# Performance work log

Measured on AMD Instinct MI355X. Metric: run time of the kernel, lower is better.

The kernel has to match this reference:

```python
import jax, jax.numpy as jnp
import numpy as np

N = 4096
IN_F = 256
OUT_F = 64
H = 4
NEG_SLOPE = 0.2


def setup_inputs() -> dict:
    key = jax.random.key(0)
    k1, k2, k3, k4 = jax.random.split(key, 4)
    x = jax.random.normal(k1, (N, IN_F), dtype=jnp.float32)
    adj = jax.random.randint(k2, (N, N), 0, 2).astype(jnp.float32)
    # Xavier-uniform init, matching nn.init.xavier_uniform_
    limW = float(np.sqrt(6.0 / (IN_F + OUT_F)))
    W = jax.random.uniform(k3, (H, IN_F, OUT_F), minval=-limW, maxval=limW, dtype=jnp.float32)
    lima = float(np.sqrt(6.0 / (2 * OUT_F + 1)))
    a = jax.random.uniform(k4, (H, 2 * OUT_F, 1), minval=-lima, maxval=lima, dtype=jnp.float32)
    return {"x": x, "adj": adj, "W": W, "a": a}


def reference(x, adj, W, a):
    # x: [N, in], adj: [N, N], W: [H, in, out], a: [H, 2*out, 1]
    n = x.shape[0]
    h, _, fo = W.shape
    Wh = jnp.einsum('nd,hdo->nho', x, W)  # [N, H, O]
    # Additive score: a^T [Wh_i || Wh_j] = (a_src . Wh_i) + (a_dst . Wh_j)
    a_src = a[:, :fo, 0]   # [H, O]
    a_dst = a[:, fo:, 0]   # [H, O]
    s_i = jnp.einsum('nho,ho->nh', Wh, a_src)  # [N, H]
    s_j = jnp.einsum('nho,ho->nh', Wh, a_dst)  # [N, H]
    e = jax.nn.leaky_relu(s_i[:, None, :] + s_j[None, :, :], NEG_SLOPE)  # [N, N, H]
    # Add self-loops on the diagonal, mask non-edges
    idx = jnp.arange(n)
    adj_sl = adj.at[idx, idx].set(1.0)
    mask = (adj_sl != 0)[:, :, None]  # [N, N, 1]
    e_masked = jnp.where(mask, e, -jnp.inf)
    attention = jax.nn.softmax(e_masked, axis=1)  # softmax over neighbors j
    # (dropout is identity in eval mode)
    h_prime = jnp.einsum('ijh,jho->iho', attention, Wh)  # [N, H, O]
    return h_prime.reshape(n, h * fo)  # concat=True
```

## Files before the change

### kernel.cpp

```cpp
#include <hip/hip_runtime.h>
#include <hip/hip_bf16.h>

typedef float    f32x4 __attribute__((ext_vector_type(4)));
typedef _Float16 f16x8 __attribute__((ext_vector_type(8)));
typedef _Float16 f16x4 __attribute__((ext_vector_type(4)));
typedef __fp16   fp16x2 __attribute__((ext_vector_type(2)));

#define NN 4096
#define INF_ 256
#define OUTF 64
#define NH 4
#define NSPL 8
#define NGRP 128
#define LOG2E 1.4426950408889634f

__global__ __launch_bounds__(256) void k0_pack(const float* __restrict__ adj,
                                               unsigned* __restrict__ pack,
                                               unsigned* __restrict__ smax)
{
    const int r    = blockIdx.x;
    const int w    = threadIdx.x >> 6;
    const int lane = threadIdx.x & 63;
    const float* row = adj + (size_t)r * NN + w * 1024;
#pragma unroll
    for (int i = 0; i < 4; ++i) {
        float a0 = row[i*256 + lane];
        float a1 = row[i*256 +  64 + lane];
        float a2 = row[i*256 + 128 + lane];
        float a3 = row[i*256 + 192 + lane];
        unsigned long long bal[4];
        bal[0] = __ballot(a0 != 0.f);
        bal[1] = __ballot(a1 != 0.f);
        bal[2] = __ballot(a2 != 0.f);
        bal[3] = __ballot(a3 != 0.f);
        if (lane < 2) {
#pragma unroll
            for (int k = 0; k < 4; ++k) {
                int wi = w*32 + i*8 + k*2 + lane;
                unsigned v = (unsigned)(bal[k] >> (lane * 32));
                if (wi == (r >> 5)) v |= 1u << (r & 31);
                pack[r*128 + wi] = v;
            }
        }
    }
    if (r == 0 && threadIdx.x < NH) smax[threadIdx.x] = 0u;
}

__device__ __forceinline__ unsigned enc_f32(float f) {
    unsigned u = __float_as_uint(f);
    return (u & 0x80000000u) ? ~u : (u | 0x80000000u);
}
__device__ __forceinline__ float dec_f32(unsigned u) {
    return (u & 0x80000000u) ? __uint_as_float(u ^ 0x80000000u)
                             : __uint_as_float(~u);
}

__global__ __launch_bounds__(256) void kW_tr(const float* __restrict__ W,
                                             _Float16* __restrict__ wBh,
                                             _Float16* __restrict__ wBl)
{
    const int b = blockIdx.x;
    const int h = b >> 3, ks = b & 7;
    const int t = threadIdx.x;
    const int ob = t >> 6, lane = t & 63;
    const int row16 = lane & 15, quad = lane >> 4;

    const float* wp = W + (size_t)h*INF_*OUTF + (ks*32 + quad*8)*OUTF + ob*16 + row16;
    f16x8 vh, vl;
#pragma unroll
    for (int e = 0; e < 8; ++e) {
        float v = wp[e*OUTF];
        _Float16 hi = (_Float16)v;
        vh[e] = hi;
        vl[e] = (_Float16)(v - (float)hi);
    }
    const int idx = ((h*8 + ks)*4 + ob)*64 + lane;
    reinterpret_cast<f16x8*>(wBh)[idx] = vh;
    reinterpret_cast<f16x8*>(wBl)[idx] = vl;
}

__global__ __launch_bounds__(256) void k1m(
    const float* __restrict__ x, const _Float16* __restrict__ wBh,
    const _Float16* __restrict__ wBl, const float* __restrict__ a,
    _Float16* __restrict__ whB, float* __restrict__ s_src,
    float* __restrict__ s_dst, unsigned* __restrict__ smax)
{
    const int b = blockIdx.x;
    const int h = b >> 6, rb = b & 63;
    const int w = threadIdx.x >> 6, lane = threadIdx.x & 63;
    const int row16 = lane & 15, quad = lane >> 4;
    const int n0 = rb*64 + w*16;

    f32x4 acc[4];
#pragma unroll
    for (int ob = 0; ob < 4; ++ob) acc[ob] = (f32x4){0,0,0,0};

    const float* xp = x + (size_t)(n0 + row16)*INF_ + quad*8;
    const f16x8* WH = reinterpret_cast<const f16x8*>(wBh) + (h*8*4)*64 + lane;
    const f16x8* WL = reinterpret_cast<const f16x8*>(wBl) + (h*8*4)*64 + lane;

#pragma unroll
    for (int ks = 0; ks < 8; ++ks) {
        float4 xv0 = *reinterpret_cast<const float4*>(xp + ks*32);
        float4 xv1 = *reinterpret_cast<const float4*>(xp + ks*32 + 4);
        const float xv[8] = {xv0.x,xv0.y,xv0.z,xv0.w,xv1.x,xv1.y,xv1.z,xv1.w};
        f16x8 Ah, Al;
#pragma unroll
        for (int e = 0; e < 8; ++e) {
            _Float16 hi = (_Float16)xv[e];
            Ah[e] = hi;
            Al[e] = (_Float16)(xv[e] - (float)hi);
        }
#pragma unroll
        for (int ob = 0; ob < 4; ++ob) {
            f16x8 bh = WH[(ks*4 + ob)*64];
            f16x8 bl = WL[(ks*4 + ob)*64];
            acc[ob] = __builtin_amdgcn_mfma_f32_16x16x32_f16(Ah, bh, acc[ob], 0, 0, 0);
            acc[ob] = __builtin_amdgcn_mfma_f32_16x16x32_f16(Al, bh, acc[ob], 0, 0, 0);
            acc[ob] = __builtin_amdgcn_mfma_f32_16x16x32_f16(Ah, bl, acc[ob], 0, 0, 0);
        }
    }

    {
        const int jblk = n0 >> 5;
        const int qb   = ((n0 & 16) >> 3) + (quad >> 1);
        const int e0   = (quad & 1) * 4;
#pragma unroll
        for (int ob = 0; ob < 4; ++ob) {
            f16x4 st;
#pragma unroll
            for (int q = 0; q < 4; ++q) st[q] = (_Float16)acc[ob][q];
            const size_t off = (((size_t)(h*NGRP + jblk)*4 + ob)*64 + qb*16 + row16)*8 + e0;
            *reinterpret_cast<f16x4*>(whB + off) = st;
        }
    }

    float asv[4], adv[4];
#pragma unroll
    for (int ob = 0; ob < 4; ++ob) {
        asv[ob] = a[h*128 + ob*16 + row16];
        adv[ob] = a[h*128 + 64 + ob*16 + row16];
    }
    float sq_s[4], sq_d[4];
#pragma unroll
    for (int q = 0; q < 4; ++q) {
        float vs = 0.f, vd = 0.f;
#pragma unroll
        for (int ob = 0; ob < 4; ++ob) {
            vs += acc[ob][q] * asv[ob];
            vd += acc[ob][q] * adv[ob];
        }
#pragma unroll
        for (int m = 1; m <= 8; m <<= 1) {
            vs += __shfl_xor(vs, m);
            vd += __shfl_xor(vd, m);
        }
        sq_s[q] = vs; sq_d[q] = vd;
    }
    if (row16 == 0) {
        float vmax = -3.0e38f;
#pragma unroll
        for (int q = 0; q < 4; ++q) {
            const int n = n0 + quad*4 + q;
            s_src[h*NN + n] = LOG2E * sq_s[q];
            const float sd = LOG2E * sq_d[q];
            s_dst[h*NN + n] = sd;
            vmax = fmaxf(vmax, sd);
        }
        atomicMax(&smax[h], enc_f32(vmax));
    }
}

template <int USE_PART>
__global__ __launch_bounds__(256, 4) void k3_attn(
    const unsigned* __restrict__ pack, const _Float16* __restrict__ whB,
    const float* __restrict__ s_src, const float* __restrict__ s_dst,
    const unsigned* __restrict__ smax_enc,
    float* __restrict__ outp, float* __restrict__ l_ws)
{
    constexpr int STEPS_ = NN / NSPL / 32;

    const int b      = blockIdx.x;
    const int jsplit = b % NSPL;
    const int r2     = b / NSPL;
    const int hh     = r2 & 3;
    const int grp    = r2 >> 2;
    const int w      = threadIdx.x >> 6;
    const int lane   = threadIdx.x & 63;
    const int row16  = lane & 15;
    const int quad   = lane >> 4;
    const int i0     = (grp * 4 + w) * 32;
    const int jb0    = jsplit * (NN / NSPL);
    const int jblk0  = jb0 >> 5;

    const float sm = dec_f32(smax_enc[hh]);
    float A1[2], A2[2];
    const unsigned* prow[2];
#pragma unroll
    for (int f = 0; f < 2; ++f) {
        const int ir = i0 + f*16 + row16;
        const float s_i = s_src[hh*NN + ir];
        const float zb  = s_i + sm;
        const float mb  = fmaxf(zb, 0.2f * zb);
        A1[f] = s_i - mb;
        A2[f] = 0.2f * s_i - mb;
        prow[f] = pack + ir*128 + jblk0;
    }

    f32x4 acc[2][4];
    f32x4 accl[2];
#pragma unroll
    for (int f = 0; f < 2; ++f) {
        accl[f] = (f32x4){0,0,0,0};
#pragma unroll
        for (int ob = 0; ob < 4; ++ob) acc[f][ob] = (f32x4){0,0,0,0};
    }

    f16x8 ones;
#pragma unroll
    for (int e = 0; e < 8; ++e) ones[e] = (_Float16)1.0f;

    const _Float16* bB  = whB + (size_t)(hh*NGRP + jblk0)*2048 + lane*8;
    const float*    sdp = s_dst + hh*NN + jb0 + quad*8;

    f16x8 B0 = *reinterpret_cast<const f16x8*>(bB);
    f16x8 B1 = *reinterpret_cast<const f16x8*>(bB + 512);
    f16x8 B2 = *reinterpret_cast<const f16x8*>(bB + 1024);
    f16x8 B3 = *reinterpret_cast<const f16x8*>(bB + 1536);
    unsigned msk0 = prow[0][0], msk1 = prow[1][0];
    float4 sj0 = *reinterpret_cast<const float4*>(sdp);
    float4 sj1 = *reinterpret_cast<const float4*>(sdp + 4);

    for (int s = 0; s < STEPS_; ++s) {
        const _Float16* bn = bB + (s+1)*2048;
        f16x8 nB0 = *reinterpret_cast<const f16x8*>(bn);
        f16x8 nB1 = *reinterpret_cast<const f16x8*>(bn + 512);
        f16x8 nB2 = *reinterpret_cast<const f16x8*>(bn + 1024);
        f16x8 nB3 = *reinterpret_cast<const f16x8*>(bn + 1536);
        unsigned nmsk0 = prow[0][s+1], nmsk1 = prow[1][s+1];
        float4 nsj0 = *reinterpret_cast<const float4*>(sdp + (s+1)*32);
        float4 nsj1 = *reinterpret_cast<const float4*>(sdp + (s+1)*32 + 4);

        const float sjv[8] = {sj0.x,sj0.y,sj0.z,sj0.w,sj1.x,sj1.y,sj1.z,sj1.w};
        float us[8];
#pragma unroll
        for (int e = 0; e < 8; ++e) us[e] = 0.2f * sjv[e];

        const unsigned mskf[2] = {msk0, msk1};
#pragma unroll
        for (int f = 0; f < 2; ++f) {
            const unsigned mm8 = (mskf[f] >> (quad * 8)) & 0xffu;
            float pe[8];
#pragma unroll
            for (int e = 0; e < 8; ++e) {
                float t1 = A1[f] + sjv[e];
                float t2 = A2[f] + us[e];
                float p  = __builtin_amdgcn_exp2f(fmaxf(t1, t2));
                pe[e] = (mm8 & (1u << e)) ? p : 0.0f;
            }
            union { f16x8 v8; fp16x2 p2[4]; } pa;
#pragma unroll
            for (int e2 = 0; e2 < 4; ++e2)
                pa.p2[e2] = __builtin_amdgcn_cvt_pkrtz(pe[2*e2], pe[2*e2+1]);

            acc[f][0] = __builtin_amdgcn_mfma_f32_16x16x32_f16(pa.v8, B0, acc[f][0], 0, 0, 0);
            acc[f][1] = __builtin_amdgcn_mfma_f32_16x16x32_f16(pa.v8, B1, acc[f][1], 0, 0, 0);
            acc[f][2] = __builtin_amdgcn_mfma_f32_16x16x32_f16(pa.v8, B2, acc[f][2], 0, 0, 0);
            acc[f][3] = __builtin_amdgcn_mfma_f32_16x16x32_f16(pa.v8, B3, acc[f][3], 0, 0, 0);
            accl[f]   = __builtin_amdgcn_mfma_f32_16x16x32_f16(pa.v8, ones, accl[f], 0, 0, 0);
        }

        B0 = nB0; B1 = nB1; B2 = nB2; B3 = nB3;
        msk0 = nmsk0; msk1 = nmsk1;
        sj0 = nsj0; sj1 = nsj1;
    }

#pragma unroll
    for (int f = 0; f < 2; ++f) {
        if (row16 == 0) {
#pragma unroll
            for (int q = 0; q < 4; ++q) {
                const int ir = i0 + f*16 + quad*4 + q;
                if (USE_PART) l_ws[(jsplit*NH + hh)*NN + ir] = accl[f][q];
                else          atomicAdd(&l_ws[hh*NN + ir], accl[f][q]);
            }
        }
    }
    if (USE_PART) {
        float* pw = outp + ((size_t)((jsplit*NH + hh)*NGRP + (i0 >> 5))) * 2048 + lane;
#pragma unroll
        for (int f = 0; f < 2; ++f)
#pragma unroll
            for (int ob = 0; ob < 4; ++ob)
#pragma unroll
                for (int q = 0; q < 4; ++q)
                    pw[((f*4 + ob)*4 + q)*64] = acc[f][ob][q];
    } else {
#pragma unroll
        for (int f = 0; f < 2; ++f)
#pragma unroll
            for (int ob = 0; ob < 4; ++ob)
#pragma unroll
                for (int q = 0; q < 4; ++q) {
                    const int grow = i0 + f*16 + quad*4 + q;
                    const int gcol = hh*OUTF + ob*16 + row16;
                    atomicAdd(&outp[(size_t)grow*256 + gcol], acc[f][ob][q]);
                }
    }
}

__global__ __launch_bounds__(256) void k4_part(const float* __restrict__ part,
                                               const float* __restrict__ l_ws,
                                               float* __restrict__ out)
{
    const int idx = blockIdx.x * 256 + threadIdx.x;
    const int n = idx >> 6, c4 = idx & 63;
    const int h = c4 >> 4, k = c4 & 15;
    const int g = n >> 5, f = (n >> 4) & 1, quad = (n >> 2) & 3, q = n & 3;
    const int ob = k >> 2, lb = quad*16 + (k & 3)*4;

    float L = 0.f;
    f32x4 v = {0,0,0,0};
#pragma unroll
    for (int sp = 0; sp < NSPL; ++sp) {
        L += l_ws[(sp*NH + h)*NN + n];
        const float* p = part + ((size_t)((sp*NH + h)*NGRP + g))*2048
                              + ((f*4 + ob)*4 + q)*64 + lb;
        v += *reinterpret_cast<const f32x4*>(p);
    }
    const float inv = 1.0f / L;
    *reinterpret_cast<f32x4*>(out + (size_t)n*256 + c4*4) = v * inv;
}

__global__ __launch_bounds__(256) void k4_atomic(float* __restrict__ out,
                                                 const float* __restrict__ l_acc)
{
    const int idx = blockIdx.x * 256 + threadIdx.x;
    const int n = idx >> 6, c4 = idx & 63, h = c4 >> 4;
    const float inv = 1.0f / l_acc[h*NN + n];
    f32x4 v = *reinterpret_cast<f32x4*>(out + (size_t)n*256 + c4*4);
    *reinterpret_cast<f32x4*>(out + (size_t)n*256 + c4*4) = v * inv;
}

extern "C" void kernel_launch(void* const* d_in, const int* in_sizes, int n_in,
                              void* d_out, int out_size, void* d_ws, size_t ws_size,
                              hipStream_t stream)
{
    const float* x   = (const float*)d_in[0];
    const float* adj = (const float*)d_in[1];
    const float* W   = (const float*)d_in[2];
    const float* a   = (const float*)d_in[3];
    float* out = (float*)d_out;

    char* ws = (char*)d_ws;
    _Float16* whB  = (_Float16*)ws;
    unsigned* pack = (unsigned*)(ws + (2u<<20));
    _Float16* wBh  = (_Float16*)(ws + (4u<<20));
    _Float16* wBl  = (_Float16*)(ws + (4u<<20) + (128u<<10));
    float* s_src   = (float*)(ws + (4u<<20) + (256u<<10));
    float* s_dst   = (float*)(ws + (4u<<20) + (320u<<10));
    unsigned* smax = (unsigned*)(ws + (4u<<20) + (384u<<10));
    float* l_ws    = (float*)(ws + (4u<<20) + (385u<<10));
    float* part    = (float*)(ws + (4u<<20) + (897u<<10));

    const size_t need = (4u<<20) + (897u<<10) + (size_t)NSPL * NN * 256 * 4;

    k0_pack<<<NN, 256, 0, stream>>>(adj, pack, smax);
    kW_tr  <<<32, 256, 0, stream>>>(W, wBh, wBl);
    k1m    <<<256, 256, 0, stream>>>(x, wBh, wBl, a, whB, s_src, s_dst, smax);

    if (ws_size >= need) {
        k3_attn<1><<<1024, 256, 0, stream>>>(pack, whB, s_src, s_dst, smax, part, l_ws);
        k4_part<<<1024, 256, 0, stream>>>(part, l_ws, out);
    } else {
        (void)hipMemsetAsync(d_out, 0, (size_t)out_size * sizeof(float), stream);
        (void)hipMemsetAsync(l_ws, 0, NH * NN * sizeof(float), stream);
        k3_attn<0><<<1024, 256, 0, stream>>>(pack, whB, s_src, s_dst, smax, out, l_ws);
        k4_atomic<<<1024, 256, 0, stream>>>(out, l_ws);
    }
}
```

Before: 81.03 us.

## Split projection kernel across output blocks and store split partials as fp16

The projection kernel now gives each wave one 16-column output block instead of four, launching 1024 blocks instead of 256. The attention scores are reduced across waves through shared memory with a block barrier. Separately, the per-split partial outputs are packed to fp16 with round-toward-zero conversion, halving the workspace traffic between the attention and combine kernels. This adds precision loss in unnormalized partial sums and extra x reloads per wave.

```diff
diff --git a/kernel.cpp b/kernel.cpp
--- a/kernel.cpp
+++ b/kernel.cpp
@@ -85,19 +85,20 @@
     _Float16* __restrict__ whB, float* __restrict__ s_src,
     float* __restrict__ s_dst, unsigned* __restrict__ smax)
 {
+    __shared__ float red_s[4][16];
+    __shared__ float red_d[4][16];
+
     const int b = blockIdx.x;
-    const int h = b >> 6, rb = b & 63;
-    const int w = threadIdx.x >> 6, lane = threadIdx.x & 63;
+    const int h = b >> 8, g = b & 255;
+    const int n0 = g * 16;
+    const int ob = threadIdx.x >> 6;
+    const int lane = threadIdx.x & 63;
     const int row16 = lane & 15, quad = lane >> 4;
-    const int n0 = rb*64 + w*16;
-
-    f32x4 acc[4];
-#pragma unroll
-    for (int ob = 0; ob < 4; ++ob) acc[ob] = (f32x4){0,0,0,0};
-
+
+    f32x4 acc = {0,0,0,0};
     const float* xp = x + (size_t)(n0 + row16)*INF_ + quad*8;
-    const f16x8* WH = reinterpret_cast<const f16x8*>(wBh) + (h*8*4)*64 + lane;
-    const f16x8* WL = reinterpret_cast<const f16x8*>(wBl) + (h*8*4)*64 + lane;
+    const f16x8* WH = reinterpret_cast<const f16x8*>(wBh) + h*2048 + ob*64 + lane;
+    const f16x8* WL = reinterpret_cast<const f16x8*>(wBl) + h*2048 + ob*64 + lane;
 
 #pragma unroll
     for (int ks = 0; ks < 8; ++ks) {
@@ -111,63 +112,52 @@
             Ah[e] = hi;
             Al[e] = (_Float16)(xv[e] - (float)hi);
         }
-#pragma unroll
-        for (int ob = 0; ob < 4; ++ob) {
-            f16x8 bh = WH[(ks*4 + ob)*64];
-            f16x8 bl = WL[(ks*4 + ob)*64];
-            acc[ob] = __builtin_amdgcn_mfma_f32_16x16x32_f16(Ah, bh, acc[ob], 0, 0, 0);
-            acc[ob] = __builtin_amdgcn_mfma_f32_16x16x32_f16(Al, bh, acc[ob], 0, 0, 0);
-            acc[ob] = __builtin_amdgcn_mfma_f32_16x16x32_f16(Ah, bl, acc[ob], 0, 0, 0);
-        }
+        f16x8 bh = WH[ks*256];
+        f16x8 bl = WL[ks*256];
+        acc = __builtin_amdgcn_mfma_f32_16x16x32_f16(Ah, bh, acc, 0, 0, 0);
+        acc = __builtin_amdgcn_mfma_f32_16x16x32_f16(Al, bh, acc, 0, 0, 0);
+        acc = __builtin_amdgcn_mfma_f32_16x16x32_f16(Ah, bl, acc, 0, 0, 0);
     }
 
     {
         const int jblk = n0 >> 5;
         const int qb   = ((n0 & 16) >> 3) + (quad >> 1);
         const int e0   = (quad & 1) * 4;
-#pragma unroll
-        for (int ob = 0; ob < 4; ++ob) {
-            f16x4 st;
-#pragma unroll
-            for (int q = 0; q < 4; ++q) st[q] = (_Float16)acc[ob][q];
-            const size_t off = (((size_t)(h*NGRP + jblk)*4 + ob)*64 + qb*16 + row16)*8 + e0;
-            *reinterpret_cast<f16x4*>(whB + off) = st;
-        }
-    }
-
-    float asv[4], adv[4];
-#pragma unroll
-    for (int ob = 0; ob < 4; ++ob) {
-        asv[ob] = a[h*128 + ob*16 + row16];
-        adv[ob] = a[h*128 + 64 + ob*16 + row16];
-    }
-    float sq_s[4], sq_d[4];
+        f16x4 st;
+#pragma unroll
+        for (int q = 0; q < 4; ++q) st[q] = (_Float16)acc[q];
+        const size_t off = (((size_t)(h*NGRP + jblk)*4 + ob)*64 + qb*16 + row16)*8 + e0;
+        *reinterpret_cast<f16x4*>(whB + off) = st;
+    }
+
+    const float as = a[h*128 + ob*16 + row16];
+    const float ad = a[h*128 + 64 + ob*16 + row16];
 #pragma unroll
     for (int q = 0; q < 4; ++q) {
-        float vs = 0.f, vd = 0.f;
-#pragma unroll
-        for (int ob = 0; ob < 4; ++ob) {
-            vs += acc[ob][q] * asv[ob];
-            vd += acc[ob][q] * adv[ob];
-        }
+        float vs = acc[q] * as;
+        float vd = acc[q] * ad;
 #pragma unroll
         for (int m = 1; m <= 8; m <<= 1) {
             vs += __shfl_xor(vs, m);
             vd += __shfl_xor(vd, m);
         }
-        sq_s[q] = vs; sq_d[q] = vd;
-    }
-    if (row16 == 0) {
-        float vmax = -3.0e38f;
-#pragma unroll
-        for (int q = 0; q < 4; ++q) {
-            const int n = n0 + quad*4 + q;
-            s_src[h*NN + n] = LOG2E * sq_s[q];
-            const float sd = LOG2E * sq_d[q];
-            s_dst[h*NN + n] = sd;
-            vmax = fmaxf(vmax, sd);
-        }
-        atomicMax(&smax[h], enc_f32(vmax));
+        if (row16 == 0) {
+            red_s[ob][quad*4 + q] = vs;
+            red_d[ob][quad*4 + q] = vd;
+        }
+    }
+    __syncthreads();
+    if (threadIdx.x < 16) {
+        const int r = threadIdx.x;
+        const float vs = red_s[0][r] + red_s[1][r] + red_s[2][r] + red_s[3][r];
+        const float vd = red_d[0][r] + red_d[1][r] + red_d[2][r] + red_d[3][r];
+        const float sd = LOG2E * vd;
+        s_src[h*NN + n0 + r] = LOG2E * vs;
+        s_dst[h*NN + n0 + r] = sd;
+        float vmax = sd;
+#pragma unroll
+        for (int m = 1; m <= 8; m <<= 1) vmax = fmaxf(vmax, __shfl_xor(vmax, m));
+        if (r == 0) atomicMax(&smax[h], enc_f32(vmax));
     }
 }
 
@@ -287,14 +277,18 @@
         }
     }
     if (USE_PART) {
-        float* pw = outp + ((size_t)((jsplit*NH + hh)*NGRP + (i0 >> 5))) * 2048 + lane;
+        unsigned* pw = reinterpret_cast<unsigned*>(outp)
+                     + ((size_t)((jsplit*NH + hh)*NGRP + (i0 >> 5))) * 1024 + lane;
 #pragma unroll
         for (int f = 0; f < 2; ++f)
 #pragma unroll
-            for (int ob = 0; ob < 4; ++ob)
-#pragma unroll
-                for (int q = 0; q < 4; ++q)
-                    pw[((f*4 + ob)*4 + q)*64] = acc[f][ob][q];
+            for (int ob = 0; ob < 4; ++ob) {
+                union { fp16x2 h2; unsigned u; } p0, p1;
+                p0.h2 = __builtin_amdgcn_cvt_pkrtz(acc[f][ob][0], acc[f][ob][1]);
+                p1.h2 = __builtin_amdgcn_cvt_pkrtz(acc[f][ob][2], acc[f][ob][3]);
+                pw[((f*4 + ob)*2 + 0)*64] = p0.u;
+                pw[((f*4 + ob)*2 + 1)*64] = p1.u;
+            }
     } else {
 #pragma unroll
         for (int f = 0; f < 2; ++f)
@@ -309,7 +303,7 @@
     }
 }
 
-__global__ __launch_bounds__(256) void k4_part(const float* __restrict__ part,
+__global__ __launch_bounds__(256) void k4_part(const unsigned* __restrict__ part,
                                                const float* __restrict__ l_ws,
                                                float* __restrict__ out)
 {
@@ -318,15 +312,18 @@
     const int h = c4 >> 4, k = c4 & 15;
     const int g = n >> 5, f = (n >> 4) & 1, quad = (n >> 2) & 3, q = n & 3;
     const int ob = k >> 2, lb = quad*16 + (k & 3)*4;
+    const int wi = ((f*4 + ob)*2 + (q >> 1))*64 + lb;
+    const int hsel = q & 1;
 
     float L = 0.f;
     f32x4 v = {0,0,0,0};
 #pragma unroll
     for (int sp = 0; sp < NSPL; ++sp) {
         L += l_ws[(sp*NH + h)*NN + n];
-        const float* p = part + ((size_t)((sp*NH + h)*NGRP + g))*2048
-                              + ((f*4 + ob)*4 + q)*64 + lb;
-        v += *reinterpret_cast<const f32x4*>(p);
+        union { uint4 u4; _Float16 hx[8]; } uu;
+        uu.u4 = *reinterpret_cast<const uint4*>(part + ((size_t)((sp*NH + h)*NGRP + g))*1024 + wi);
+#pragma unroll
+        for (int i = 0; i < 4; ++i) v[i] += (float)uu.hx[i*2 + hsel];
     }
     const float inv = 1.0f / L;
     *reinterpret_cast<f32x4*>(out + (size_t)n*256 + c4*4) = v * inv;
@@ -361,17 +358,18 @@
     float* s_dst   = (float*)(ws + (4u<<20) + (320u<<10));
     unsigned* smax = (unsigned*)(ws + (4u<<20) + (384u<<10));
     float* l_ws    = (float*)(ws + (4u<<20) + (385u<<10));
-    float* part    = (float*)(ws + (4u<<20) + (897u<<10));
-
-    const size_t need = (4u<<20) + (897u<<10) + (size_t)NSPL * NN * 256 * 4;
+    char*  partb   = ws + (4u<<20) + (897u<<10);
+
+    const size_t need = (4u<<20) + (897u<<10) + (size_t)NSPL * NN * 256 * 2;
 
     k0_pack<<<NN, 256, 0, stream>>>(adj, pack, smax);
     kW_tr  <<<32, 256, 0, stream>>>(W, wBh, wBl);
-    k1m    <<<256, 256, 0, stream>>>(x, wBh, wBl, a, whB, s_src, s_dst, smax);
+    k1m    <<<1024, 256, 0, stream>>>(x, wBh, wBl, a, whB, s_src, s_dst, smax);
 
     if (ws_size >= need) {
-        k3_attn<1><<<1024, 256, 0, stream>>>(pack, whB, s_src, s_dst, smax, part, l_ws);
-        k4_part<<<1024, 256, 0, stream>>>(part, l_ws, out);
+        k3_attn<1><<<1024, 256, 0, stream>>>(pack, whB, s_src, s_dst, smax,
+                                             (float*)partb, l_ws);
+        k4_part<<<1024, 256, 0, stream>>>((const unsigned*)partb, l_ws, out);
     } else {
         (void)hipMemsetAsync(d_out, 0, (size_t)out_size * sizeof(float), stream);
         (void)hipMemsetAsync(l_ws, 0, NH * NN * sizeof(float), stream);
```

Measured after the change: 101.7 us. 25.5% more time.
